# Optimization experiments

Hardware: AMD Instinct MI355X
Metric: run time of the kernel (lower is better)

Reference implementation:

```python
import jax, jax.numpy as jnp
import numpy as np

D_MODEL = 1024
N_HEADS = 16
HEAD_DIM = D_MODEL // N_HEADS


def setup_inputs() -> dict:
    key = jax.random.key(0)
    ks = jax.random.split(key, 9)
    B, T = 2, 2048
    s = 1.0 / np.sqrt(D_MODEL)
    x = jax.random.normal(ks[0], (B, T, D_MODEL), dtype=jnp.float32)
    Wq = jax.random.uniform(ks[1], (D_MODEL, D_MODEL), jnp.float32, -s, s)
    bq = jax.random.uniform(ks[2], (D_MODEL,), jnp.float32, -s, s)
    Wk = jax.random.uniform(ks[3], (D_MODEL, D_MODEL), jnp.float32, -s, s)
    bk = jax.random.uniform(ks[4], (D_MODEL,), jnp.float32, -s, s)
    Wv = jax.random.uniform(ks[5], (D_MODEL, D_MODEL), jnp.float32, -s, s)
    bv = jax.random.uniform(ks[6], (D_MODEL,), jnp.float32, -s, s)
    Wp = jax.random.uniform(ks[7], (D_MODEL, D_MODEL), jnp.float32, -s, s)
    bp = jax.random.uniform(ks[8], (D_MODEL,), jnp.float32, -s, s)
    return {"x": x, "Wq": Wq, "bq": bq, "Wk": Wk, "bk": bk,
            "Wv": Wv, "bv": bv, "Wp": Wp, "bp": bp}


def reference(x, Wq, bq, Wk, bk, Wv, bv, Wp, bp):
    B, T, C = x.shape
    H, Dh = N_HEADS, HEAD_DIM
    # torch Linear: x @ W.T + b
    q = (x @ Wq.T + bq).reshape(B, T, H, Dh).transpose(0, 2, 1, 3)  # [B,H,T,Dh]
    k = (x @ Wk.T + bk).reshape(B, T, H, Dh).transpose(0, 2, 1, 3)
    v = (x @ Wv.T + bv).reshape(B, T, H, Dh).transpose(0, 2, 1, 3)
    scale = 1.0 / np.sqrt(Dh).astype(np.float32)
    att = jnp.einsum('bhqd,bhkd->bhqk', q, k) * scale  # [B,H,T,T]
    causal = jnp.tril(jnp.ones((T, T), dtype=bool))
    att = jnp.where(causal[None, None], att, -jnp.inf)
    att = jax.nn.softmax(att, axis=-1)
    y = jnp.einsum('bhqk,bhkd->bhqd', att, v)  # [B,H,T,Dh]
    y = y.transpose(0, 2, 1, 3).reshape(B, T, C)
    return y @ Wp.T + bp
```

## Files before the change

### kernel.cpp

```cpp
#include <hip/hip_runtime.h>
#include <hip/hip_bf16.h>
#include <math.h>

#define D_MODEL 1024
#define N_HEADS 16
#define HEAD_DIM 64
#define SEQ_T 2048
#define BATCH 2

typedef __attribute__((ext_vector_type(8))) short short8;
typedef __attribute__((ext_vector_type(4))) float f32x4;

__device__ __forceinline__ unsigned short f2bf(float f) {
    union { float f; unsigned int u; } v; v.f = f;
    return (unsigned short)((v.u + 0x7FFFu + ((v.u >> 16) & 1u)) >> 16);
}

__device__ __forceinline__ void glds16(const unsigned short* g, unsigned short* l) {
    __builtin_amdgcn_global_load_lds(
        (const __attribute__((address_space(1))) unsigned int*)g,
        (__attribute__((address_space(3))) unsigned int*)l, 16, 0, 0);
}

__global__ void cvt_all(const float4* __restrict__ x,
                        const float4* __restrict__ Wq, const float4* __restrict__ Wk,
                        const float4* __restrict__ Wv, const float4* __restrict__ Wp,
                        ushort4* __restrict__ xb, ushort4* __restrict__ wb,
                        ushort4* __restrict__ wpb) {
    int i = blockIdx.x * 256 + threadIdx.x;
    float4 v; ushort4* dst;
    if (i < 1048576) { v = x[i]; dst = xb + i; }
    else {
        int j = i - 1048576;
        int wsel = j >> 18;
        int o = j & 262143;
        const float4* s = wsel == 0 ? Wq : wsel == 1 ? Wk : wsel == 2 ? Wv : Wp;
        v = s[o];
        dst = (wsel == 3) ? (wpb + o) : (wb + (size_t)wsel * 262144 + o);
    }
    ushort4 u;
    u.x = f2bf(v.x); u.y = f2bf(v.y); u.z = f2bf(v.z); u.w = f2bf(v.w);
    *dst = u;
}

template<int MODE, int MTILE>
__global__ __launch_bounds__(256) void gemm2(
    const unsigned short* __restrict__ A,
    const unsigned short* __restrict__ W,
    const float* __restrict__ b0, const float* __restrict__ b1, const float* __restrict__ b2,
    void* __restrict__ o0, void* __restrict__ o1, void* __restrict__ o2)
{
    constexpr int K = 1024;
    constexpr int MT = MTILE / 32;
    constexpr int CAW = MTILE / 64;
    __shared__ unsigned short As[MTILE * 32];
    __shared__ unsigned short Bs[128 * 32];
    const int m0 = blockIdx.y * MTILE;
    const int n0 = blockIdx.x * 128;
    const int tid = threadIdx.x;
    const int w = tid >> 6, lane = tid & 63;
    const int col = lane & 15, quad = lane >> 4;
    const int wm = (w & 1) * (MTILE / 2), wn = (w >> 1) * 64;
    const int lr = lane >> 2, lc = (lane & 3) * 8;

    const f32x4 zero = {0.f, 0.f, 0.f, 0.f};
    f32x4 acc[MT][4];
#pragma unroll
    for (int i = 0; i < MT; i++)
#pragma unroll
        for (int j = 0; j < 4; j++) acc[i][j] = zero;

    for (int k0 = 0; k0 < K; k0 += 32) {
        __syncthreads();
#pragma unroll
        for (int c = 0; c < CAW; c++) {
            const int q = w * CAW + c;
            glds16(&A[(size_t)(m0 + q * 16 + lr) * K + k0 + lc], &As[q * 512]);
        }
#pragma unroll
        for (int c = 0; c < 2; c++) {
            const int q = w * 2 + c;
            glds16(&W[(size_t)(n0 + q * 16 + lr) * K + k0 + lc], &Bs[q * 512]);
        }
        __syncthreads();
        short8 af[MT], bf[4];
#pragma unroll
        for (int mt = 0; mt < MT; mt++)
            af[mt] = *(const short8*)&As[(wm + mt * 16 + col) * 32 + quad * 8];
#pragma unroll
        for (int nt = 0; nt < 4; nt++)
            bf[nt] = *(const short8*)&Bs[(wn + nt * 16 + col) * 32 + quad * 8];
#pragma unroll
        for (int mt = 0; mt < MT; mt++)
#pragma unroll
            for (int nt = 0; nt < 4; nt++)
                acc[mt][nt] = __builtin_amdgcn_mfma_f32_16x16x32_bf16(af[mt], bf[nt], acc[mt][nt], 0, 0, 0);
    }

#pragma unroll
    for (int mt = 0; mt < MT; mt++) {
#pragma unroll
        for (int nt = 0; nt < 4; nt++) {
            const int n = n0 + wn + nt * 16 + col;
            float bias;
            if constexpr (MODE == 2) bias = b0[n];
            else {
                const int sel = n >> 10, nq = n & 1023;
                bias = (sel == 0 ? b0 : sel == 1 ? b1 : b2)[nq];
            }
#pragma unroll
            for (int r = 0; r < 4; r++) {
                const int m = m0 + wm + mt * 16 + quad * 4 + r;
                const float v = acc[mt][nt][r] + bias;
                if constexpr (MODE == 2) {
                    ((float*)o0)[(size_t)m * 1024 + n] = v;
                } else {
                    const int sel = n >> 10, nq = n & 1023;
                    const int h = nq >> 6, dh = nq & 63, b = m >> 11, t = m & 2047;
                    if (sel < 2) {
                        unsigned short* dst = sel ? (unsigned short*)o1 : (unsigned short*)o0;
                        int tt = t;
                        if (sel == 1) {
                            const int tb = t & 31;
                            tt = (t & ~31) + ((tb & 4) << 2) + ((tb >> 3) << 2) + (tb & 3);
                        }
                        dst[(((size_t)(b * N_HEADS + h)) * SEQ_T + tt) * HEAD_DIM + dh] = f2bf(v);
                    } else {
                        ((unsigned short*)o2)[((size_t)(b * N_HEADS + h) * HEAD_DIM + dh) * SEQ_T + t] = f2bf(v);
                    }
                }
            }
        }
    }
}

__global__ __launch_bounds__(256) void flash9(
    const unsigned short* __restrict__ Q,
    const unsigned short* __restrict__ Kp,
    const unsigned short* __restrict__ Vt,
    unsigned short* __restrict__ Y)
{
    __shared__ unsigned short Ks[2][64 * 64];
    __shared__ unsigned short Vs[2][64 * 64];

    const int tid = threadIdx.x;
    const int w = tid >> 6, lane = tid & 63;
    const int col = lane & 15, quad = lane >> 4;
    const int i = blockIdx.x;
    const int bh = (i & 7) * 4 + ((i >> 3) & 3);
    const int sp = i >> 5;
    const int b = bh >> 4, h = bh & 15;

    const unsigned short* qbase = Q + (size_t)bh * SEQ_T * HEAD_DIM;
    const unsigned short* kbase = Kp + (size_t)bh * SEQ_T * HEAD_DIM;
    const unsigned short* vbase = Vt + (size_t)bh * HEAD_DIM * SEQ_T;

    const int srow = lane >> 3;
    const int schunk = (lane & 7) ^ srow;
    const int cswz = col & 7;

    const float SC2 = 0.18033688011f;
    const f32x4 zero = {0.f, 0.f, 0.f, 0.f};

    for (int ti = 0; ti < 2; ti++) {
        const int s = ti ? (15 - sp) : sp;
        const int qrow = s * 128 + w * 32;
        short8 qf[2][2];
#pragma unroll
        for (int m = 0; m < 2; m++) {
            qf[m][0] = *(const short8*)&qbase[(size_t)(qrow + m * 16 + col) * HEAD_DIM + quad * 8];
            qf[m][1] = *(const short8*)&qbase[(size_t)(qrow + m * 16 + col) * HEAD_DIM + quad * 8 + 32];
        }

        f32x4 acc[2][4];
#pragma unroll
        for (int m = 0; m < 2; m++)
#pragma unroll
            for (int nt = 0; nt < 4; nt++) acc[m][nt] = zero;
        float l[2] = {0.f, 0.f};

        const int nk = 2 * s + 2;

        __syncthreads();
#pragma unroll
        for (int rq = 0; rq < 2; rq++) {
            const int rr = rq * 32 + 8 * w;
            glds16(&kbase[(size_t)(rr + srow) * HEAD_DIM + schunk * 8], &Ks[0][rr * 64]);
            glds16(&vbase[(size_t)(rr + srow) * SEQ_T + schunk * 8], &Vs[0][rr * 64]);
        }

        int cur = 0;
        for (int kt = 0; kt < nk; kt++) {
            const int kb = kt * 64;
            __syncthreads();

            if (kt + 1 < nk) {
                const int kb2 = kb + 64;
#pragma unroll
                for (int rq = 0; rq < 2; rq++) {
                    const int rr = rq * 32 + 8 * w;
                    glds16(&kbase[(size_t)(kb2 + rr + srow) * HEAD_DIM + schunk * 8], &Ks[cur ^ 1][rr * 64]);
                    glds16(&vbase[(size_t)(rr + srow) * SEQ_T + kb2 + schunk * 8], &Vs[cur ^ 1][rr * 64]);
                }
            }

            if (kb <= qrow + 31) {
                const unsigned short* ks = Ks[cur];
                const unsigned short* vs = Vs[cur];

                short8 vB[2][4];
#pragma unroll
                for (int g = 0; g < 2; g++)
#pragma unroll
                    for (int nt = 0; nt < 4; nt++)
                        vB[g][nt] = *(const short8*)&vs[(nt * 16 + col) * 64 + (((g * 4 + quad) ^ cswz) * 8)];

                f32x4 St[2][4];
                __builtin_amdgcn_s_setprio(1);
#pragma unroll
                for (int kc = 0; kc < 4; kc++) {
                    const short8 kf0 = *(const short8*)&ks[(kc * 16 + col) * 64 + ((quad ^ cswz) * 8)];
                    const short8 kf1 = *(const short8*)&ks[(kc * 16 + col) * 64 + (((quad + 4) ^ cswz) * 8)];
#pragma unroll
                    for (int m = 0; m < 2; m++) {
                        f32x4 z = zero;
                        z = __builtin_amdgcn_mfma_f32_16x16x32_bf16(kf0, qf[m][0], z, 0, 0, 0);
                        z = __builtin_amdgcn_mfma_f32_16x16x32_bf16(kf1, qf[m][1], z, 0, 0, 0);
                        St[m][kc] = z;
                    }
                }
                __builtin_amdgcn_s_setprio(0);

                const bool needMask = (kb + 63 > qrow);
#pragma unroll
                for (int m = 0; m < 2; m++) {
                    const int qq = qrow + m * 16 + col;
                    short8 pA[2];
                    if (needMask) {
#pragma unroll
                        for (int g = 0; g < 2; g++) {
                            union { short8 s; __hip_bfloat162 h[4]; } pu;
#pragma unroll
                            for (int t16 = 0; t16 < 2; t16++) {
                                const int kc = 2 * g + t16;
                                const int kbase_c = kb + (kc >> 1) * 32 + quad * 8 + (kc & 1) * 4;
                                float p[4];
#pragma unroll
                                for (int r = 0; r < 4; r++) {
                                    p[r] = __builtin_amdgcn_exp2f(St[m][kc][r] * SC2);
                                    if (kbase_c + r > qq) p[r] = 0.f;
                                    l[m] += p[r];
                                }
                                pu.h[t16 * 2]     = __float22bfloat162_rn(make_float2(p[0], p[1]));
                                pu.h[t16 * 2 + 1] = __float22bfloat162_rn(make_float2(p[2], p[3]));
                            }
                            pA[g] = pu.s;
                        }
                    } else {
#pragma unroll
                        for (int g = 0; g < 2; g++) {
                            union { short8 s; __hip_bfloat162 h[4]; } pu;
#pragma unroll
                            for (int t16 = 0; t16 < 2; t16++) {
                                const int kc = 2 * g + t16;
                                float p[4];
#pragma unroll
                                for (int r = 0; r < 4; r++) {
                                    p[r] = __builtin_amdgcn_exp2f(St[m][kc][r] * SC2);
                                    l[m] += p[r];
                                }
                                pu.h[t16 * 2]     = __float22bfloat162_rn(make_float2(p[0], p[1]));
                                pu.h[t16 * 2 + 1] = __float22bfloat162_rn(make_float2(p[2], p[3]));
                            }
                            pA[g] = pu.s;
                        }
                    }

                    __builtin_amdgcn_s_setprio(1);
#pragma unroll
                    for (int g = 0; g < 2; g++)
#pragma unroll
                        for (int nt = 0; nt < 4; nt++)
                            acc[m][nt] = __builtin_amdgcn_mfma_f32_16x16x32_bf16(pA[g], vB[g][nt], acc[m][nt], 0, 0, 0);
                    __builtin_amdgcn_s_setprio(0);
                }
            }

            cur ^= 1;
        }

#pragma unroll
        for (int m = 0; m < 2; m++) {
            float lm = l[m];
            lm += __shfl_xor(lm, 16);
            lm += __shfl_xor(lm, 32);
            const float linv = 1.0f / lm;
            float lr[4];
#pragma unroll
            for (int r = 0; r < 4; r++) lr[r] = __shfl(linv, quad * 4 + r);
#pragma unroll
            for (int nt = 0; nt < 4; nt++)
#pragma unroll
                for (int r = 0; r < 4; r++) {
                    const int qg = qrow + m * 16 + quad * 4 + r;
                    Y[((size_t)(b * SEQ_T + qg)) * D_MODEL + h * HEAD_DIM + nt * 16 + col] =
                        f2bf(acc[m][nt][r] * lr[r]);
                }
        }
    }
}

extern "C" void kernel_launch(void* const* d_in, const int* in_sizes, int n_in,
                              void* d_out, int out_size, void* d_ws, size_t ws_size,
                              hipStream_t stream) {
    const float* x  = (const float*)d_in[0];
    const float* Wq = (const float*)d_in[1];
    const float* bq = (const float*)d_in[2];
    const float* Wk = (const float*)d_in[3];
    const float* bk = (const float*)d_in[4];
    const float* Wv = (const float*)d_in[5];
    const float* bv = (const float*)d_in[6];
    const float* Wp = (const float*)d_in[7];
    const float* bp = (const float*)d_in[8];
    float* out = (float*)d_out;

    char* ws = (char*)d_ws;
    const size_t XSZ = (size_t)4096 * 1024 * 2;
    unsigned short* xb  = (unsigned short*)ws;  ws += XSZ;
    unsigned short* wb  = (unsigned short*)ws;  ws += (size_t)3072 * 1024 * 2;
    unsigned short* wpb = (unsigned short*)ws;  ws += (size_t)1024 * 1024 * 2;
    unsigned short* qb  = (unsigned short*)ws;  ws += XSZ;
    unsigned short* kb  = (unsigned short*)ws;  ws += XSZ;
    unsigned short* vtb = (unsigned short*)ws;  ws += XSZ;
    unsigned short* yb  = (unsigned short*)ws;  ws += XSZ;

    cvt_all<<<8192, 256, 0, stream>>>((const float4*)x, (const float4*)Wq, (const float4*)Wk,
                                      (const float4*)Wv, (const float4*)Wp,
                                      (ushort4*)xb, (ushort4*)wb, (ushort4*)wpb);

    gemm2<3, 128><<<dim3(24, 32), 256, 0, stream>>>(xb, wb, bq, bk, bv, qb, kb, vtb);

    flash9<<<256, 256, 0, stream>>>(qb, kb, vtb, yb);

    gemm2<2, 64><<<dim3(8, 64), 256, 0, stream>>>(yb, wpb, bp, nullptr, nullptr, out, nullptr, nullptr);
}
```

Before: 195.0 us.

## Split flash attention into 64-row query tiles with 2-wave blocks

Replaces the 256-thread flash kernel, where each block walked two 128-row query tiles paired for causal balance, with 1024 blocks of 128 threads that each own one 64-row query tile. Tiles are assigned in four groups that pair short and long causal rows. Each wave now skips no key tiles, and only the last (diagonal) tile is masked. This gives more blocks for finer load balance and occupancy. The cost is loading more K/V per query row, since tiles are shared by 2 waves instead of 4, and more blocks.

```diff
diff --git a/kernel.cpp b/kernel.cpp
--- a/kernel.cpp
+++ b/kernel.cpp
@@ -134,7 +134,7 @@
     }
 }
 
-__global__ __launch_bounds__(256) void flash9(
+__global__ __launch_bounds__(128) void flash10(
     const unsigned short* __restrict__ Q,
     const unsigned short* __restrict__ Kp,
     const unsigned short* __restrict__ Vt,
@@ -147,8 +147,11 @@
     const int w = tid >> 6, lane = tid & 63;
     const int col = lane & 15, quad = lane >> 4;
     const int i = blockIdx.x;
-    const int bh = (i & 7) * 4 + ((i >> 3) & 3);
-    const int sp = i >> 5;
+    const int g = i & 255, r4 = i >> 8;
+    const int bh = (g & 7) * 4 + ((g >> 3) & 3);
+    const int q0 = g >> 5;
+    const int qt = (r4 == 0) ? q0 : (r4 == 1) ? (31 - q0)
+                 : (r4 == 2) ? (q0 + 8) : (23 - q0);
     const int b = bh >> 4, h = bh & 15;
 
     const unsigned short* qbase = Q + (size_t)bh * SEQ_T * HEAD_DIM;
@@ -162,151 +165,145 @@
     const float SC2 = 0.18033688011f;
     const f32x4 zero = {0.f, 0.f, 0.f, 0.f};
 
-    for (int ti = 0; ti < 2; ti++) {
-        const int s = ti ? (15 - sp) : sp;
-        const int qrow = s * 128 + w * 32;
-        short8 qf[2][2];
+    const int qrow = qt * 64 + w * 32;
+    short8 qf[2][2];
+#pragma unroll
+    for (int m = 0; m < 2; m++) {
+        qf[m][0] = *(const short8*)&qbase[(size_t)(qrow + m * 16 + col) * HEAD_DIM + quad * 8];
+        qf[m][1] = *(const short8*)&qbase[(size_t)(qrow + m * 16 + col) * HEAD_DIM + quad * 8 + 32];
+    }
+
+    f32x4 acc[2][4];
+#pragma unroll
+    for (int m = 0; m < 2; m++)
+#pragma unroll
+        for (int nt = 0; nt < 4; nt++) acc[m][nt] = zero;
+    float l[2] = {0.f, 0.f};
+
+    const int nk = qt + 1;
+
+#pragma unroll
+    for (int rq = 0; rq < 4; rq++) {
+        const int rr = rq * 16 + 8 * w;
+        glds16(&kbase[(size_t)(rr + srow) * HEAD_DIM + schunk * 8], &Ks[0][rr * 64]);
+        glds16(&vbase[(size_t)(rr + srow) * SEQ_T + schunk * 8], &Vs[0][rr * 64]);
+    }
+
+    int cur = 0;
+    for (int kt = 0; kt < nk; kt++) {
+        const int kb = kt * 64;
+        __syncthreads();
+
+        if (kt + 1 < nk) {
+            const int kb2 = kb + 64;
+#pragma unroll
+            for (int rq = 0; rq < 4; rq++) {
+                const int rr = rq * 16 + 8 * w;
+                glds16(&kbase[(size_t)(kb2 + rr + srow) * HEAD_DIM + schunk * 8], &Ks[cur ^ 1][rr * 64]);
+                glds16(&vbase[(size_t)(rr + srow) * SEQ_T + kb2 + schunk * 8], &Vs[cur ^ 1][rr * 64]);
+            }
+        }
+
+        const unsigned short* ks = Ks[cur];
+        const unsigned short* vs = Vs[cur];
+
+        short8 vB[2][4];
+#pragma unroll
+        for (int gg = 0; gg < 2; gg++)
+#pragma unroll
+            for (int nt = 0; nt < 4; nt++)
+                vB[gg][nt] = *(const short8*)&vs[(nt * 16 + col) * 64 + (((gg * 4 + quad) ^ cswz) * 8)];
+
+        f32x4 St[2][4];
+        __builtin_amdgcn_s_setprio(1);
+#pragma unroll
+        for (int kc = 0; kc < 4; kc++) {
+            const short8 kf0 = *(const short8*)&ks[(kc * 16 + col) * 64 + ((quad ^ cswz) * 8)];
+            const short8 kf1 = *(const short8*)&ks[(kc * 16 + col) * 64 + (((quad + 4) ^ cswz) * 8)];
+#pragma unroll
+            for (int m = 0; m < 2; m++) {
+                f32x4 z = zero;
+                z = __builtin_amdgcn_mfma_f32_16x16x32_bf16(kf0, qf[m][0], z, 0, 0, 0);
+                z = __builtin_amdgcn_mfma_f32_16x16x32_bf16(kf1, qf[m][1], z, 0, 0, 0);
+                St[m][kc] = z;
+            }
+        }
+        __builtin_amdgcn_s_setprio(0);
+
+        const bool diag = (kt == nk - 1);
 #pragma unroll
         for (int m = 0; m < 2; m++) {
-            qf[m][0] = *(const short8*)&qbase[(size_t)(qrow + m * 16 + col) * HEAD_DIM + quad * 8];
-            qf[m][1] = *(const short8*)&qbase[(size_t)(qrow + m * 16 + col) * HEAD_DIM + quad * 8 + 32];
-        }
-
-        f32x4 acc[2][4];
-#pragma unroll
-        for (int m = 0; m < 2; m++)
-#pragma unroll
-            for (int nt = 0; nt < 4; nt++) acc[m][nt] = zero;
-        float l[2] = {0.f, 0.f};
-
-        const int nk = 2 * s + 2;
-
-        __syncthreads();
-#pragma unroll
-        for (int rq = 0; rq < 2; rq++) {
-            const int rr = rq * 32 + 8 * w;
-            glds16(&kbase[(size_t)(rr + srow) * HEAD_DIM + schunk * 8], &Ks[0][rr * 64]);
-            glds16(&vbase[(size_t)(rr + srow) * SEQ_T + schunk * 8], &Vs[0][rr * 64]);
-        }
-
-        int cur = 0;
-        for (int kt = 0; kt < nk; kt++) {
-            const int kb = kt * 64;
-            __syncthreads();
-
-            if (kt + 1 < nk) {
-                const int kb2 = kb + 64;
-#pragma unroll
-                for (int rq = 0; rq < 2; rq++) {
-                    const int rr = rq * 32 + 8 * w;
-                    glds16(&kbase[(size_t)(kb2 + rr + srow) * HEAD_DIM + schunk * 8], &Ks[cur ^ 1][rr * 64]);
-                    glds16(&vbase[(size_t)(rr + srow) * SEQ_T + kb2 + schunk * 8], &Vs[cur ^ 1][rr * 64]);
+            const int qq = qrow + m * 16 + col;
+            short8 pA[2];
+            if (diag) {
+#pragma unroll
+                for (int gg = 0; gg < 2; gg++) {
+                    union { short8 s; __hip_bfloat162 h[4]; } pu;
+#pragma unroll
+                    for (int t16 = 0; t16 < 2; t16++) {
+                        const int kc = 2 * gg + t16;
+                        const int kbase_c = kb + (kc >> 1) * 32 + quad * 8 + (kc & 1) * 4;
+                        float p[4];
+#pragma unroll
+                        for (int r = 0; r < 4; r++) {
+                            p[r] = __builtin_amdgcn_exp2f(St[m][kc][r] * SC2);
+                            if (kbase_c + r > qq) p[r] = 0.f;
+                            l[m] += p[r];
+                        }
+                        pu.h[t16 * 2]     = __float22bfloat162_rn(make_float2(p[0], p[1]));
+                        pu.h[t16 * 2 + 1] = __float22bfloat162_rn(make_float2(p[2], p[3]));
+                    }
+                    pA[gg] = pu.s;
                 }
-            }
-
-            if (kb <= qrow + 31) {
-                const unsigned short* ks = Ks[cur];
-                const unsigned short* vs = Vs[cur];
-
-                short8 vB[2][4];
-#pragma unroll
-                for (int g = 0; g < 2; g++)
-#pragma unroll
-                    for (int nt = 0; nt < 4; nt++)
-                        vB[g][nt] = *(const short8*)&vs[(nt * 16 + col) * 64 + (((g * 4 + quad) ^ cswz) * 8)];
-
-                f32x4 St[2][4];
-                __builtin_amdgcn_s_setprio(1);
-#pragma unroll
-                for (int kc = 0; kc < 4; kc++) {
-                    const short8 kf0 = *(const short8*)&ks[(kc * 16 + col) * 64 + ((quad ^ cswz) * 8)];
-                    const short8 kf1 = *(const short8*)&ks[(kc * 16 + col) * 64 + (((quad + 4) ^ cswz) * 8)];
-#pragma unroll
-                    for (int m = 0; m < 2; m++) {
-                        f32x4 z = zero;
-                        z = __builtin_amdgcn_mfma_f32_16x16x32_bf16(kf0, qf[m][0], z, 0, 0, 0);
-                        z = __builtin_amdgcn_mfma_f32_16x16x32_bf16(kf1, qf[m][1], z, 0, 0, 0);
-                        St[m][kc] = z;
+            } else {
+#pragma unroll
+                for (int gg = 0; gg < 2; gg++) {
+                    union { short8 s; __hip_bfloat162 h[4]; } pu;
+#pragma unroll
+                    for (int t16 = 0; t16 < 2; t16++) {
+                        const int kc = 2 * gg + t16;
+                        float p[4];
+#pragma unroll
+                        for (int r = 0; r < 4; r++) {
+                            p[r] = __builtin_amdgcn_exp2f(St[m][kc][r] * SC2);
+                            l[m] += p[r];
+                        }
+                        pu.h[t16 * 2]     = __float22bfloat162_rn(make_float2(p[0], p[1]));
+                        pu.h[t16 * 2 + 1] = __float22bfloat162_rn(make_float2(p[2], p[3]));
                     }
+                    pA[gg] = pu.s;
                 }
-                __builtin_amdgcn_s_setprio(0);
-
-                const bool needMask = (kb + 63 > qrow);
-#pragma unroll
-                for (int m = 0; m < 2; m++) {
-                    const int qq = qrow + m * 16 + col;
-                    short8 pA[2];
-                    if (needMask) {
-#pragma unroll
-                        for (int g = 0; g < 2; g++) {
-                            union { short8 s; __hip_bfloat162 h[4]; } pu;
-#pragma unroll
-                            for (int t16 = 0; t16 < 2; t16++) {
-                                const int kc = 2 * g + t16;
-                                const int kbase_c = kb + (kc >> 1) * 32 + quad * 8 + (kc & 1) * 4;
-                                float p[4];
-#pragma unroll
-                                for (int r = 0; r < 4; r++) {
-                                    p[r] = __builtin_amdgcn_exp2f(St[m][kc][r] * SC2);
-                                    if (kbase_c + r > qq) p[r] = 0.f;
-                                    l[m] += p[r];
-                                }
-                                pu.h[t16 * 2]     = __float22bfloat162_rn(make_float2(p[0], p[1]));
-                                pu.h[t16 * 2 + 1] = __float22bfloat162_rn(make_float2(p[2], p[3]));
-                            }
-                            pA[g] = pu.s;
-                        }
-                    } else {
-#pragma unroll
-                        for (int g = 0; g < 2; g++) {
-                            union { short8 s; __hip_bfloat162 h[4]; } pu;
-#pragma unroll
-                            for (int t16 = 0; t16 < 2; t16++) {
-                                const int kc = 2 * g + t16;
-                                float p[4];
-#pragma unroll
-                                for (int r = 0; r < 4; r++) {
-                                    p[r] = __builtin_amdgcn_exp2f(St[m][kc][r] * SC2);
-                                    l[m] += p[r];
-                                }
-                                pu.h[t16 * 2]     = __float22bfloat162_rn(make_float2(p[0], p[1]));
-                                pu.h[t16 * 2 + 1] = __float22bfloat162_rn(make_float2(p[2], p[3]));
-                            }
-                            pA[g] = pu.s;
-                        }
-                    }
-
-                    __builtin_amdgcn_s_setprio(1);
-#pragma unroll
-                    for (int g = 0; g < 2; g++)
-#pragma unroll
-                        for (int nt = 0; nt < 4; nt++)
-                            acc[m][nt] = __builtin_amdgcn_mfma_f32_16x16x32_bf16(pA[g], vB[g][nt], acc[m][nt], 0, 0, 0);
-                    __builtin_amdgcn_s_setprio(0);
-                }
-            }
-
-            cur ^= 1;
-        }
-
-#pragma unroll
-        for (int m = 0; m < 2; m++) {
-            float lm = l[m];
-            lm += __shfl_xor(lm, 16);
-            lm += __shfl_xor(lm, 32);
-            const float linv = 1.0f / lm;
-            float lr[4];
-#pragma unroll
-            for (int r = 0; r < 4; r++) lr[r] = __shfl(linv, quad * 4 + r);
-#pragma unroll
-            for (int nt = 0; nt < 4; nt++)
-#pragma unroll
-                for (int r = 0; r < 4; r++) {
-                    const int qg = qrow + m * 16 + quad * 4 + r;
-                    Y[((size_t)(b * SEQ_T + qg)) * D_MODEL + h * HEAD_DIM + nt * 16 + col] =
-                        f2bf(acc[m][nt][r] * lr[r]);
-                }
-        }
+            }
+
+            __builtin_amdgcn_s_setprio(1);
+#pragma unroll
+            for (int gg = 0; gg < 2; gg++)
+#pragma unroll
+                for (int nt = 0; nt < 4; nt++)
+                    acc[m][nt] = __builtin_amdgcn_mfma_f32_16x16x32_bf16(pA[gg], vB[gg][nt], acc[m][nt], 0, 0, 0);
+            __builtin_amdgcn_s_setprio(0);
+        }
+
+        cur ^= 1;
+    }
+
+#pragma unroll
+    for (int m = 0; m < 2; m++) {
+        float lm = l[m];
+        lm += __shfl_xor(lm, 16);
+        lm += __shfl_xor(lm, 32);
+        const float linv = 1.0f / lm;
+        float lr[4];
+#pragma unroll
+        for (int r = 0; r < 4; r++) lr[r] = __shfl(linv, quad * 4 + r);
+#pragma unroll
+        for (int nt = 0; nt < 4; nt++)
+#pragma unroll
+            for (int r = 0; r < 4; r++) {
+                const int qg = qrow + m * 16 + quad * 4 + r;
+                Y[((size_t)(b * SEQ_T + qg)) * D_MODEL + h * HEAD_DIM + nt * 16 + col] =
+                    f2bf(acc[m][nt][r] * lr[r]);
+            }
     }
 }
 
@@ -340,7 +337,7 @@
 
     gemm2<3, 128><<<dim3(24, 32), 256, 0, stream>>>(xb, wb, bq, bk, bv, qb, kb, vtb);
 
-    flash9<<<256, 256, 0, stream>>>(qb, kb, vtb, yb);
+    flash10<<<1024, 128, 0, stream>>>(qb, kb, vtb, yb);
 
     gemm2<2, 64><<<dim3(8, 64), 256, 0, stream>>>(yb, wpb, bp, nullptr, nullptr, out, nullptr, nullptr);
 }
```

Result: no change. 192.2 us (-1.4%).
